# Kernel tuning notes

Measured on AMD Instinct MI355X. Metric: run time of the kernel, lower is better.

The kernel has to match this reference:

```python
import jax, jax.numpy as jnp
import numpy as np

INPUT_DIM = 1024
UNITS = 1024

def setup_inputs() -> dict:
    key = jax.random.key(0)
    ks = jax.random.split(key, 7)
    B, S = 4, 2048
    x = jax.random.normal(ks[0], (B, S, INPUT_DIM), dtype=jnp.float32)
    # nn.Linear weights stored as [out, in]; biases [out]
    scale = 1.0 / np.sqrt(INPUT_DIM)
    Wq = jax.random.uniform(ks[1], (UNITS, INPUT_DIM), jnp.float32, -scale, scale)
    bq = jax.random.uniform(ks[2], (UNITS,), jnp.float32, -scale, scale)
    Wk = jax.random.uniform(ks[3], (UNITS, INPUT_DIM), jnp.float32, -scale, scale)
    bk = jax.random.uniform(ks[4], (UNITS,), jnp.float32, -scale, scale)
    Wv = jax.random.uniform(ks[5], (UNITS, INPUT_DIM), jnp.float32, -scale, scale)
    bv = jax.random.uniform(ks[6], (UNITS,), jnp.float32, -scale, scale)
    return {"x": x, "Wq": Wq, "bq": bq, "Wk": Wk, "bk": bk, "Wv": Wv, "bv": bv}

def reference(x, Wq, bq, Wk, bk, Wv, bv):
    # Q/K/V projections: [B,S,D] @ [D,U]
    Q = jnp.einsum('bsd,ud->bsu', x, Wq) + bq
    K = jnp.einsum('bsd,ud->bsu', x, Wk) + bk
    V = jnp.einsum('bsd,ud->bsu', x, Wv) + bv
    scores = jnp.einsum('bqu,bku->bqk', Q, K) / jnp.sqrt(jnp.float32(UNITS))
    attn = jax.nn.softmax(scores, axis=-1)
    return jnp.einsum('bqk,bku->bqu', attn, V)
```

## Files before the change

### kernel.cpp

```cpp
#include <hip/hip_runtime.h>
#include <cstdint>
#include <cstddef>


typedef unsigned short ushort_t;
typedef unsigned char u8;
typedef __attribute__((ext_vector_type(4))) short short4v;
typedef __attribute__((ext_vector_type(8))) short short8;
typedef __attribute__((ext_vector_type(4))) float f32x4;

#define AS1 __attribute__((address_space(1)))
#define AS3 __attribute__((address_space(3)))

__device__ __forceinline__ ushort_t f2bf(float f) {
    unsigned int u = __float_as_uint(f);
    u += 0x7FFFu + ((u >> 16) & 1u);
    return (ushort_t)(u >> 16);
}
__device__ __forceinline__ float bf2f(ushort_t b) {
    return __uint_as_float(((unsigned)b) << 16);
}

__device__ __forceinline__ void async_ld16(const void* g, unsigned lds_off) {
    __builtin_amdgcn_global_load_lds((const AS1 void*)(uintptr_t)g,
                                     (AS3 void*)(uintptr_t)lds_off,
                                     16, 0, 0);
}

__global__ __launch_bounds__(512, 2) void qkv_gemm(
    const ushort_t* __restrict__ X,
    const ushort_t* __restrict__ W0, const ushort_t* __restrict__ W1,
    const ushort_t* __restrict__ W2,
    const float* __restrict__ b0, const float* __restrict__ b1,
    const float* __restrict__ b2,
    u8* __restrict__ Q8, u8* __restrict__ K8, ushort_t* __restrict__ Vt)
{
    __shared__ __align__(16) ushort_t As[128 * 64];
    __shared__ __align__(16) ushort_t Bs[3][128 * 64];

    const int tid  = threadIdx.x;
    const int wave = tid >> 6;
    const int lane = tid & 63;

    const int m0 = blockIdx.y * 128;
    const int n0 = blockIdx.x * 128;
    const int wm = (wave >> 2) * 64;
    const int wn = (wave & 3) * 32;

    const unsigned ldsA = (unsigned)(uintptr_t)&As[0];
    const unsigned ldsB = (unsigned)(uintptr_t)&Bs[0][0];
    constexpr unsigned BSTEP = 128 * 64 * 2;

    const int srow = (wave << 3) + (lane >> 3);
    const int cd   = ((lane & 7) - (lane >> 3)) & 7;
    const ushort_t* gX  = X  + (size_t)(m0 + srow) * 1024 + cd * 8;
    const ushort_t* gW0 = W0 + (size_t)(n0 + srow) * 1024 + cd * 8;
    const ushort_t* gW1 = W1 + (size_t)(n0 + srow) * 1024 + cd * 8;
    const ushort_t* gW2 = W2 + (size_t)(n0 + srow) * 1024 + cd * 8;
    const unsigned lw = (wave << 10);

    const int frow = lane & 15;
    const int fg   = lane >> 4;

    f32x4 acc[3][4][2] = {};

    for (int k0 = 0; k0 < 1024; k0 += 64) {
        if (k0) __syncthreads();
#pragma unroll
        for (int c = 0; c < 2; ++c) {
            const size_t ro = (size_t)c * 64;
            async_ld16(gX  + ro * 1024, ldsA + c * 8192 + lw);
            async_ld16(gW0 + ro * 1024, ldsB + 0 * BSTEP + c * 8192 + lw);
            async_ld16(gW1 + ro * 1024, ldsB + 1 * BSTEP + c * 8192 + lw);
            async_ld16(gW2 + ro * 1024, ldsB + 2 * BSTEP + c * 8192 + lw);
        }
        gX += 64; gW0 += 64; gW1 += 64; gW2 += 64;
        __syncthreads();

#pragma unroll
        for (int t = 0; t < 2; ++t) {
            const int ck = (t << 2) + fg;
            short8 af[4], bf[2];
#pragma unroll
            for (int i = 0; i < 4; ++i) {
                const int row = wm + i * 16 + frow;
                af[i] = *(const short8*)&As[row * 64 + (((ck + row) & 7) << 3)];
            }
#pragma unroll
            for (int o = 0; o < 3; ++o) {
#pragma unroll
                for (int j = 0; j < 2; ++j) {
                    const int row = wn + j * 16 + frow;
                    bf[j] = *(const short8*)&Bs[o][row * 64 + (((ck + row) & 7) << 3)];
                }
#pragma unroll
                for (int i = 0; i < 4; ++i)
#pragma unroll
                    for (int j = 0; j < 2; ++j)
                        acc[o][i][j] = __builtin_amdgcn_mfma_f32_16x16x32_bf16(
                            af[i], bf[j], acc[o][i][j], 0, 0, 0);
            }
        }
    }

    const int r0 = (lane >> 4) << 2;
    const int c0 = lane & 15;
#pragma unroll
    for (int o = 0; o < 2; ++o) {
        u8* C = (o == 0) ? Q8 : K8;
        const float* bia = (o == 0) ? b0 : b1;
#pragma unroll
        for (int i = 0; i < 4; ++i) {
#pragma unroll
            for (int j = 0; j < 2; ++j) {
                const int n = n0 + wn + j * 16 + c0;
                const float bn = bia[n];
                const int p0 = __builtin_amdgcn_cvt_pk_fp8_f32(
                    acc[o][i][j][0] + bn, acc[o][i][j][1] + bn, 0, false);
                const int p1 = __builtin_amdgcn_cvt_pk_fp8_f32(
                    acc[o][i][j][2] + bn, acc[o][i][j][3] + bn, 0, false);
                const size_t mb = (size_t)(m0 + wm + i * 16 + r0);
                C[(mb + 0) * 1024 + n] = (u8)(p0 & 0xFF);
                C[(mb + 1) * 1024 + n] = (u8)((p0 >> 8) & 0xFF);
                C[(mb + 2) * 1024 + n] = (u8)(p1 & 0xFF);
                C[(mb + 3) * 1024 + n] = (u8)((p1 >> 8) & 0xFF);
            }
        }
    }
#pragma unroll
    for (int i = 0; i < 4; ++i) {
#pragma unroll
        for (int j = 0; j < 2; ++j) {
            const int n = n0 + wn + j * 16 + c0;
            const int m = m0 + wm + i * 16 + r0;
            const float bn = b2[n];
            short4v pk;
#pragma unroll
            for (int r = 0; r < 4; ++r)
                pk[r] = (short)f2bf(acc[2][i][j][r] + bn);
            *(short4v*)&Vt[(size_t)n * 8192 + m] = pk;
        }
    }
}

__global__ __launch_bounds__(256, 2) void qk_fp8(
    const u8* __restrict__ Q8, const u8* __restrict__ K8,
    ushort_t* __restrict__ Sc)
{
    __shared__ __align__(16) u8 As[128 * 64];
    __shared__ __align__(16) u8 Bs[128 * 64];

    const int tid  = threadIdx.x;
    const int wave = tid >> 6;
    const int lane = tid & 63;

    const u8* A = Q8 + (size_t)blockIdx.z * 2048 * 1024;
    const u8* B = K8 + (size_t)blockIdx.z * 2048 * 1024;

    const int m0 = blockIdx.y * 128;
    const int n0 = blockIdx.x * 128;
    const int wm = (wave >> 1) * 64;
    const int wn = (wave & 1) * 64;

    const unsigned ldsA = (unsigned)(uintptr_t)&As[0];
    const unsigned ldsB = (unsigned)(uintptr_t)&Bs[0];

    const int srow = (wave << 4) + (lane >> 2);
    const int cd   = ((lane & 3) - srow) & 3;
    const u8* gA = A + (size_t)(m0 + srow) * 1024 + cd * 16;
    const u8* gB = B + (size_t)(n0 + srow) * 1024 + cd * 16;
    const unsigned lw = (wave << 10);

    const int frow = lane & 15;
    const int fg   = lane >> 4;

    f32x4 acc[4][4] = {};

    for (int k0 = 0; k0 < 1024; k0 += 64) {
        if (k0) __syncthreads();
        async_ld16(gA,             ldsA + lw);
        async_ld16(gA + 64 * 1024, ldsA + 4096 + lw);
        async_ld16(gB,             ldsB + lw);
        async_ld16(gB + 64 * 1024, ldsB + 4096 + lw);
        gA += 64; gB += 64;
        __syncthreads();

#pragma unroll
        for (int t = 0; t < 2; ++t) {
            const int ck = (t << 1) + (fg >> 1);
            const int io = (fg & 1) << 3;
            long long af[4], bf[4];
#pragma unroll
            for (int i = 0; i < 4; ++i) {
                const int row = wm + i * 16 + frow;
                af[i] = *(const long long*)&As[row * 64 + (((ck + row) & 3) << 4) + io];
            }
#pragma unroll
            for (int j = 0; j < 4; ++j) {
                const int row = wn + j * 16 + frow;
                bf[j] = *(const long long*)&Bs[row * 64 + (((ck + row) & 3) << 4) + io];
            }
#pragma unroll
            for (int i = 0; i < 4; ++i)
#pragma unroll
                for (int j = 0; j < 4; ++j)
                    acc[i][j] = __builtin_amdgcn_mfma_f32_16x16x32_fp8_fp8(
                        af[i], bf[j], acc[i][j], 0, 0, 0);
        }
    }

    const int r0 = (lane >> 4) << 2;
    const int c0 = lane & 15;
    ushort_t* C = Sc + (size_t)blockIdx.z * 2048 * 2048;
#pragma unroll
    for (int i = 0; i < 4; ++i)
#pragma unroll
        for (int j = 0; j < 4; ++j) {
            const int n = n0 + wn + j * 16 + c0;
#pragma unroll
            for (int r = 0; r < 4; ++r) {
                const int m = m0 + wm + i * 16 + r0 + r;
                C[(size_t)m * 2048 + n] = f2bf(__expf(acc[i][j][r] * 0.03125f));
            }
        }
}

__global__ __launch_bounds__(256, 2) void pv_gemm(
    const ushort_t* __restrict__ A, const ushort_t* __restrict__ B0,
    float* __restrict__ C0)
{
    constexpr int BK = 64, P = 8;

    __shared__ __align__(16) ushort_t As[128 * BK];
    __shared__ __align__(16) ushort_t Bs[128 * BK];
    __shared__ float rs[128];

    const int tid  = threadIdx.x;
    const int wave = tid >> 6;
    const int lane = tid & 63;

    A += (size_t)blockIdx.z * 2048 * 2048;
    const ushort_t* B = B0 + (size_t)blockIdx.z * 2048;

    const int m0 = blockIdx.y * 128;
    const int n0 = blockIdx.x * 128;
    const int wm = (wave >> 1) * 64;
    const int wn = (wave & 1) * 64;

    const unsigned ldsA = (unsigned)(uintptr_t)&As[0];
    const unsigned ldsB = (unsigned)(uintptr_t)&Bs[0];

    const int srow = wave * 8 + lane / P;
    const int cd   = ((lane & (P - 1)) - srow) & (P - 1);
    const ushort_t* gA = A + (size_t)(m0 + srow) * 2048 + cd * 8;
    const ushort_t* gB = B + (size_t)(n0 + srow) * 8192 + cd * 8;
    const unsigned lw = (wave << 10);

    const int frow = lane & 15;
    const int fg   = lane >> 4;

    f32x4 acc[4][4] = {};
    float rsacc[4] = {0.f, 0.f, 0.f, 0.f};

    for (int k0 = 0; k0 < 2048; k0 += BK) {
        if (k0) __syncthreads();
#pragma unroll
        for (int c = 0; c < 4; ++c) {
            const size_t ro = (size_t)c * 32;
            async_ld16(gA + ro * 2048, ldsA + c * 4096 + lw);
            async_ld16(gB + ro * 8192, ldsB + c * 4096 + lw);
        }
        gA += BK; gB += BK;
        __syncthreads();

#pragma unroll
        for (int t = 0; t < 2; ++t) {
            const int pa = (((t << 2) + fg + frow) & (P - 1)) << 3;
            short8 af[4], bf[4];
#pragma unroll
            for (int i = 0; i < 4; ++i)
                af[i] = *(const short8*)&As[(wm + i * 16 + frow) * BK + pa];
            if (wn == 0) {
#pragma unroll
                for (int i = 0; i < 4; ++i)
#pragma unroll
                    for (int e = 0; e < 8; ++e)
                        rsacc[i] += bf2f((ushort_t)af[i][e]);
            }
#pragma unroll
            for (int j = 0; j < 4; ++j)
                bf[j] = *(const short8*)&Bs[(wn + j * 16 + frow) * BK + pa];
#pragma unroll
            for (int i = 0; i < 4; ++i)
#pragma unroll
                for (int j = 0; j < 4; ++j)
                    acc[i][j] = __builtin_amdgcn_mfma_f32_16x16x32_bf16(
                        af[i], bf[j], acc[i][j], 0, 0, 0);
        }
    }

    if (wn == 0) {
#pragma unroll
        for (int i = 0; i < 4; ++i) {
            float s = rsacc[i];
            s += __shfl_xor(s, 16, 64);
            s += __shfl_xor(s, 32, 64);
            rs[wm + i * 16 + frow] = s;
        }
    }
    __syncthreads();

    const int r0 = (lane >> 4) << 2;
    const int c0 = lane & 15;
    float* C = C0 + (size_t)blockIdx.z * 2048 * 1024;
#pragma unroll
    for (int i = 0; i < 4; ++i) {
        float bm[4];
#pragma unroll
        for (int r = 0; r < 4; ++r)
            bm[r] = 1.0f / rs[wm + i * 16 + r0 + r];
#pragma unroll
        for (int j = 0; j < 4; ++j) {
            const int n = n0 + wn + j * 16 + c0;
#pragma unroll
            for (int r = 0; r < 4; ++r) {
                const int m = m0 + wm + i * 16 + r0 + r;
                C[(size_t)m * 1024 + n] = acc[i][j][r] * bm[r];
            }
        }
    }
}

__global__ __launch_bounds__(256) void cvt_all(
    const float* __restrict__ x,  const float* __restrict__ wq,
    const float* __restrict__ wk, const float* __restrict__ wv,
    ushort_t* __restrict__ xb,  ushort_t* __restrict__ wqb,
    ushort_t* __restrict__ wkb, ushort_t* __restrict__ wvb)
{
    const int b = blockIdx.x;
    const float* src; ushort_t* dst; size_t base;
    if (b < 4096)      { src = x;  dst = xb;  base = (size_t)b * 2048; }
    else if (b < 4608) { src = wq; dst = wqb; base = (size_t)(b - 4096) * 2048; }
    else if (b < 5120) { src = wk; dst = wkb; base = (size_t)(b - 4608) * 2048; }
    else               { src = wv; dst = wvb; base = (size_t)(b - 5120) * 2048; }
    const size_t i = base + threadIdx.x * 8;
    const f32x4 a = *(const f32x4*)(src + i);
    const f32x4 c = *(const f32x4*)(src + i + 4);
    short8 o;
    o[0] = (short)f2bf(a[0]); o[1] = (short)f2bf(a[1]);
    o[2] = (short)f2bf(a[2]); o[3] = (short)f2bf(a[3]);
    o[4] = (short)f2bf(c[0]); o[5] = (short)f2bf(c[1]);
    o[6] = (short)f2bf(c[2]); o[7] = (short)f2bf(c[3]);
    *(short8*)(dst + i) = o;
}

extern "C" void kernel_launch(void* const* d_in, const int* in_sizes, int n_in,
                              void* d_out, int out_size, void* d_ws, size_t ws_size,
                              hipStream_t stream)
{
    const float* x  = (const float*)d_in[0];
    const float* Wq = (const float*)d_in[1];
    const float* bq = (const float*)d_in[2];
    const float* Wk = (const float*)d_in[3];
    const float* bk = (const float*)d_in[4];
    const float* Wv = (const float*)d_in[5];
    const float* bv = (const float*)d_in[6];
    float* out = (float*)d_out;

    char* ws = (char*)d_ws;
    const size_t MB = 1ull << 20;
    ushort_t* Xb  = (ushort_t*)(ws);
    ushort_t* Wqb = (ushort_t*)(ws + 16 * MB);
    ushort_t* Wkb = (ushort_t*)(ws + 18 * MB);
    ushort_t* Wvb = (ushort_t*)(ws + 20 * MB);
    u8*       Q8  = (u8*)(ws + 32 * MB);
    u8*       K8  = (u8*)(ws + 40 * MB);
    ushort_t* Vt  = (ushort_t*)(ws + 64 * MB);
    ushort_t* Sc  = (ushort_t*)(ws);

    cvt_all<<<dim3(5632), dim3(256), 0, stream>>>(
        x, Wq, Wk, Wv, Xb, Wqb, Wkb, Wvb);

    qkv_gemm<<<dim3(8, 64), dim3(512), 0, stream>>>(
        Xb, Wqb, Wkb, Wvb, bq, bk, bv, Q8, K8, Vt);

    qk_fp8<<<dim3(16, 16, 4), dim3(256), 0, stream>>>(Q8, K8, Sc);

    pv_gemm<<<dim3(8, 16, 4), dim3(256), 0, stream>>>(Sc, Vt, out);
}
```

Measured before the change: 257.0 us.

## Merge four kernels into one persistent kernel with global atomic barriers

Replaces the four separate launches (convert, QKV GEMM, QK^T fp8, PV GEMM) with one persistent 256-block kernel that walks through the phases, separated by a software grid barrier built on an atomic counter. Tile shapes change too: QK uses 128x256 tiles and PV uses 512-thread blocks with 128x128 tiles. The aim is to remove launch gaps and tail effects between kernels. In exchange it adds barrier spin cost, limits each phase to 256 blocks (2 tiles each), and depends on all 256 blocks being co-resident, or the barrier deadlocks.

```diff
diff --git a/kernel.cpp b/kernel.cpp
--- a/kernel.cpp
+++ b/kernel.cpp
@@ -20,338 +20,342 @@
 __device__ __forceinline__ float bf2f(ushort_t b) {
     return __uint_as_float(((unsigned)b) << 16);
 }
-
 __device__ __forceinline__ void async_ld16(const void* g, unsigned lds_off) {
     __builtin_amdgcn_global_load_lds((const AS1 void*)(uintptr_t)g,
-                                     (AS3 void*)(uintptr_t)lds_off,
-                                     16, 0, 0);
-}
-
-__global__ __launch_bounds__(512, 2) void qkv_gemm(
-    const ushort_t* __restrict__ X,
-    const ushort_t* __restrict__ W0, const ushort_t* __restrict__ W1,
-    const ushort_t* __restrict__ W2,
-    const float* __restrict__ b0, const float* __restrict__ b1,
-    const float* __restrict__ b2,
-    u8* __restrict__ Q8, u8* __restrict__ K8, ushort_t* __restrict__ Vt)
+                                     (AS3 void*)(uintptr_t)lds_off, 16, 0, 0);
+}
+__device__ __forceinline__ void cvt8(const float* __restrict__ s,
+                                     ushort_t* __restrict__ d, size_t i) {
+    const f32x4 a = *(const f32x4*)(s + i);
+    const f32x4 b = *(const f32x4*)(s + i + 4);
+    short8 o;
+    o[0] = (short)f2bf(a[0]); o[1] = (short)f2bf(a[1]);
+    o[2] = (short)f2bf(a[2]); o[3] = (short)f2bf(a[3]);
+    o[4] = (short)f2bf(b[0]); o[5] = (short)f2bf(b[1]);
+    o[6] = (short)f2bf(b[2]); o[7] = (short)f2bf(b[3]);
+    *(short8*)(d + i) = o;
+}
+
+__device__ __forceinline__ void gsync(int* bar, int target) {
+    __syncthreads();
+    if (threadIdx.x == 0) {
+        __hip_atomic_fetch_add(bar, 1, __ATOMIC_RELEASE,
+                               __HIP_MEMORY_SCOPE_AGENT);
+        while (__hip_atomic_load(bar, __ATOMIC_ACQUIRE,
+                                 __HIP_MEMORY_SCOPE_AGENT) < target) {
+            __builtin_amdgcn_s_sleep(8);
+        }
+    }
+    __syncthreads();
+}
+
+__global__ __launch_bounds__(512, 4) void fa_persist(
+    const float* __restrict__ x,
+    const float* __restrict__ Wq, const float* __restrict__ bq,
+    const float* __restrict__ Wk, const float* __restrict__ bk,
+    const float* __restrict__ Wv, const float* __restrict__ bv,
+    float* __restrict__ out,
+    ushort_t* __restrict__ Xb, ushort_t* __restrict__ Wqb,
+    ushort_t* __restrict__ Wkb, ushort_t* __restrict__ Wvb,
+    u8* __restrict__ Q8, u8* __restrict__ K8,
+    ushort_t* __restrict__ Vt, ushort_t* __restrict__ Sc,
+    int* __restrict__ bar)
 {
-    __shared__ __align__(16) ushort_t As[128 * 64];
-    __shared__ __align__(16) ushort_t Bs[3][128 * 64];
+    __shared__ __align__(16) char smem[65536];
 
     const int tid  = threadIdx.x;
     const int wave = tid >> 6;
     const int lane = tid & 63;
-
-    const int m0 = blockIdx.y * 128;
-    const int n0 = blockIdx.x * 128;
-    const int wm = (wave >> 2) * 64;
-    const int wn = (wave & 3) * 32;
-
-    const unsigned ldsA = (unsigned)(uintptr_t)&As[0];
-    const unsigned ldsB = (unsigned)(uintptr_t)&Bs[0][0];
-    constexpr unsigned BSTEP = 128 * 64 * 2;
-
-    const int srow = (wave << 3) + (lane >> 3);
-    const int cd   = ((lane & 7) - (lane >> 3)) & 7;
-    const ushort_t* gX  = X  + (size_t)(m0 + srow) * 1024 + cd * 8;
-    const ushort_t* gW0 = W0 + (size_t)(n0 + srow) * 1024 + cd * 8;
-    const ushort_t* gW1 = W1 + (size_t)(n0 + srow) * 1024 + cd * 8;
-    const ushort_t* gW2 = W2 + (size_t)(n0 + srow) * 1024 + cd * 8;
-    const unsigned lw = (wave << 10);
-
+    const int blk  = blockIdx.x;
     const int frow = lane & 15;
     const int fg   = lane >> 4;
-
-    f32x4 acc[3][4][2] = {};
-
-    for (int k0 = 0; k0 < 1024; k0 += 64) {
-        if (k0) __syncthreads();
-#pragma unroll
-        for (int c = 0; c < 2; ++c) {
-            const size_t ro = (size_t)c * 64;
-            async_ld16(gX  + ro * 1024, ldsA + c * 8192 + lw);
-            async_ld16(gW0 + ro * 1024, ldsB + 0 * BSTEP + c * 8192 + lw);
-            async_ld16(gW1 + ro * 1024, ldsB + 1 * BSTEP + c * 8192 + lw);
-            async_ld16(gW2 + ro * 1024, ldsB + 2 * BSTEP + c * 8192 + lw);
+    const int r0   = (lane >> 4) << 2;
+    const int c0   = lane & 15;
+
+    {
+        const int gt = blk * 512 + tid;
+#pragma unroll
+        for (int it = 0; it < 8; ++it)
+            cvt8(x, Xb, ((size_t)gt + (size_t)it * 131072) * 8);
+        cvt8(Wq, Wqb, (size_t)gt * 8);
+        cvt8(Wk, Wkb, (size_t)gt * 8);
+        cvt8(Wv, Wvb, (size_t)gt * 8);
+    }
+    gsync(bar, 256);
+
+    {
+        ushort_t* As = (ushort_t*)smem;
+        ushort_t* Bs = (ushort_t*)(smem + 16384);
+        const unsigned ldsA = (unsigned)(uintptr_t)As;
+        const unsigned ldsB = (unsigned)(uintptr_t)Bs;
+        constexpr unsigned BSTEP = 128 * 64 * 2;
+
+        for (int ti = 0; ti < 2; ++ti) {
+            const int t  = blk + ti * 256;
+            const int bx = t & 7, by = t >> 3;
+            const int m0 = by * 128, n0 = bx * 128;
+            const int wm = (wave >> 2) * 64;
+            const int wn = (wave & 3) * 32;
+
+            const int srow = (wave << 3) + (lane >> 3);
+            const int cd   = ((lane & 7) - (lane >> 3)) & 7;
+            const ushort_t* gX  = Xb  + (size_t)(m0 + srow) * 1024 + cd * 8;
+            const ushort_t* gW0 = Wqb + (size_t)(n0 + srow) * 1024 + cd * 8;
+            const ushort_t* gW1 = Wkb + (size_t)(n0 + srow) * 1024 + cd * 8;
+            const ushort_t* gW2 = Wvb + (size_t)(n0 + srow) * 1024 + cd * 8;
+            const unsigned lw = (wave << 10);
+
+            f32x4 acc[3][4][2] = {};
+
+            for (int k0 = 0; k0 < 1024; k0 += 64) {
+                __syncthreads();
+#pragma unroll
+                for (int c = 0; c < 2; ++c) {
+                    const size_t ro = (size_t)c * 64;
+                    async_ld16(gX  + ro * 1024, ldsA + c * 8192 + lw);
+                    async_ld16(gW0 + ro * 1024, ldsB + 0 * BSTEP + c * 8192 + lw);
+                    async_ld16(gW1 + ro * 1024, ldsB + 1 * BSTEP + c * 8192 + lw);
+                    async_ld16(gW2 + ro * 1024, ldsB + 2 * BSTEP + c * 8192 + lw);
+                }
+                gX += 64; gW0 += 64; gW1 += 64; gW2 += 64;
+                __syncthreads();
+
+#pragma unroll
+                for (int tt = 0; tt < 2; ++tt) {
+                    const int ck = (tt << 2) + fg;
+                    short8 af[4], bf[2];
+#pragma unroll
+                    for (int i = 0; i < 4; ++i) {
+                        const int row = wm + i * 16 + frow;
+                        af[i] = *(const short8*)&As[row * 64 + (((ck + row) & 7) << 3)];
+                    }
+#pragma unroll
+                    for (int o = 0; o < 3; ++o) {
+#pragma unroll
+                        for (int j = 0; j < 2; ++j) {
+                            const int row = wn + j * 16 + frow;
+                            bf[j] = *(const short8*)&Bs[(size_t)o * 128 * 64 +
+                                       row * 64 + (((ck + row) & 7) << 3)];
+                        }
+#pragma unroll
+                        for (int i = 0; i < 4; ++i)
+#pragma unroll
+                            for (int j = 0; j < 2; ++j)
+                                acc[o][i][j] = __builtin_amdgcn_mfma_f32_16x16x32_bf16(
+                                    af[i], bf[j], acc[o][i][j], 0, 0, 0);
+                    }
+                }
+            }
+
+#pragma unroll
+            for (int o = 0; o < 2; ++o) {
+                u8* C = (o == 0) ? Q8 : K8;
+                const float* bia = (o == 0) ? bq : bk;
+#pragma unroll
+                for (int i = 0; i < 4; ++i) {
+#pragma unroll
+                    for (int j = 0; j < 2; ++j) {
+                        const int n = n0 + wn + j * 16 + c0;
+                        const float bn = bia[n];
+                        const int p0 = __builtin_amdgcn_cvt_pk_fp8_f32(
+                            acc[o][i][j][0] + bn, acc[o][i][j][1] + bn, 0, false);
+                        const int p1 = __builtin_amdgcn_cvt_pk_fp8_f32(
+                            acc[o][i][j][2] + bn, acc[o][i][j][3] + bn, 0, false);
+                        const size_t mb = (size_t)(m0 + wm + i * 16 + r0);
+                        C[(mb + 0) * 1024 + n] = (u8)(p0 & 0xFF);
+                        C[(mb + 1) * 1024 + n] = (u8)((p0 >> 8) & 0xFF);
+                        C[(mb + 2) * 1024 + n] = (u8)(p1 & 0xFF);
+                        C[(mb + 3) * 1024 + n] = (u8)((p1 >> 8) & 0xFF);
+                    }
+                }
+            }
+#pragma unroll
+            for (int i = 0; i < 4; ++i) {
+#pragma unroll
+                for (int j = 0; j < 2; ++j) {
+                    const int n = n0 + wn + j * 16 + c0;
+                    const int m = m0 + wm + i * 16 + r0;
+                    const float bn = bv[n];
+                    short4v pk;
+#pragma unroll
+                    for (int r = 0; r < 4; ++r)
+                        pk[r] = (short)f2bf(acc[2][i][j][r] + bn);
+                    *(short4v*)&Vt[(size_t)n * 8192 + m] = pk;
+                }
+            }
         }
-        gX += 64; gW0 += 64; gW1 += 64; gW2 += 64;
-        __syncthreads();
-
-#pragma unroll
-        for (int t = 0; t < 2; ++t) {
-            const int ck = (t << 2) + fg;
-            short8 af[4], bf[2];
+    }
+    gsync(bar, 512);
+
+    {
+        u8* As8 = (u8*)smem;
+        u8* Bs8 = (u8*)(smem + 8192);
+        const unsigned ldsA = (unsigned)(uintptr_t)As8;
+        const unsigned ldsB = (unsigned)(uintptr_t)Bs8;
+
+        for (int ti = 0; ti < 2; ++ti) {
+            const int t  = blk + ti * 256;
+            const int z  = t >> 7;
+            const int rr = t & 127;
+            const int m0 = (rr >> 3) * 128;
+            const int n0 = (rr & 7) * 256;
+            const int wm = (wave >> 2) * 64;
+            const int wn = (wave & 3) * 64;
+
+            const u8* A = Q8 + (size_t)z * 2048 * 1024;
+            const u8* B = K8 + (size_t)z * 2048 * 1024;
+
+            const int srow = (wave << 4) + (lane >> 2);
+            const int cd   = ((lane & 3) - srow) & 3;
+            const u8* gA = A + (size_t)(m0 + srow) * 1024 + cd * 16;
+            const u8* gB = B + (size_t)(n0 + srow) * 1024 + cd * 16;
+            const unsigned lw = (wave << 10);
+
+            f32x4 acc[4][4] = {};
+
+            for (int k0 = 0; k0 < 1024; k0 += 64) {
+                __syncthreads();
+                async_ld16(gA,              ldsA + lw);
+                async_ld16(gB,              ldsB + lw);
+                async_ld16(gB + 128 * 1024, ldsB + 8192 + lw);
+                gA += 64; gB += 64;
+                __syncthreads();
+
+#pragma unroll
+                for (int tt = 0; tt < 2; ++tt) {
+                    const int ck = (tt << 1) + (fg >> 1);
+                    const int io = (fg & 1) << 3;
+                    long long af[4], bf[4];
+#pragma unroll
+                    for (int i = 0; i < 4; ++i) {
+                        const int row = wm + i * 16 + frow;
+                        af[i] = *(const long long*)&As8[row * 64 + (((ck + row) & 3) << 4) + io];
+                    }
+#pragma unroll
+                    for (int j = 0; j < 4; ++j) {
+                        const int row = wn + j * 16 + frow;
+                        bf[j] = *(const long long*)&Bs8[row * 64 + (((ck + row) & 3) << 4) + io];
+                    }
+#pragma unroll
+                    for (int i = 0; i < 4; ++i)
+#pragma unroll
+                        for (int j = 0; j < 4; ++j)
+                            acc[i][j] = __builtin_amdgcn_mfma_f32_16x16x32_fp8_fp8(
+                                af[i], bf[j], acc[i][j], 0, 0, 0);
+                }
+            }
+
+            ushort_t* C = Sc + (size_t)z * 2048 * 2048;
+#pragma unroll
+            for (int i = 0; i < 4; ++i)
+#pragma unroll
+                for (int j = 0; j < 4; ++j) {
+                    const int n = n0 + wn + j * 16 + c0;
+#pragma unroll
+                    for (int r = 0; r < 4; ++r) {
+                        const int m = m0 + wm + i * 16 + r0 + r;
+                        C[(size_t)m * 2048 + n] = f2bf(__expf(acc[i][j][r] * 0.03125f));
+                    }
+                }
+        }
+    }
+    gsync(bar, 768);
+
+    {
+        ushort_t* As = (ushort_t*)smem;
+        ushort_t* Bs = (ushort_t*)(smem + 16384);
+        float*    rs = (float*)(smem + 32768);
+        const unsigned ldsA = (unsigned)(uintptr_t)As;
+        const unsigned ldsB = (unsigned)(uintptr_t)Bs;
+
+        for (int ti = 0; ti < 2; ++ti) {
+            const int t  = blk + ti * 256;
+            const int z  = t >> 7;
+            const int rr = t & 127;
+            const int m0 = (rr >> 3) * 128;
+            const int n0 = (rr & 7) * 128;
+            const int wm = (wave >> 2) * 64;
+            const int wn = (wave & 3) * 32;
+
+            const ushort_t* A = Sc + (size_t)z * 2048 * 2048;
+            const ushort_t* B = Vt + (size_t)z * 2048;
+
+            const int srow = (wave << 3) + (lane >> 3);
+            const int cd   = ((lane & 7) - (lane >> 3)) & 7;
+            const ushort_t* gA = A + (size_t)(m0 + srow) * 2048 + cd * 8;
+            const ushort_t* gB = B + (size_t)(n0 + srow) * 8192 + cd * 8;
+            const unsigned lw = (wave << 10);
+
+            f32x4 acc[4][2] = {};
+            float rsacc[4] = {0.f, 0.f, 0.f, 0.f};
+
+            for (int k0 = 0; k0 < 2048; k0 += 64) {
+                __syncthreads();
+#pragma unroll
+                for (int c = 0; c < 2; ++c) {
+                    const size_t ro = (size_t)c * 64;
+                    async_ld16(gA + ro * 2048, ldsA + c * 8192 + lw);
+                    async_ld16(gB + ro * 8192, ldsB + c * 8192 + lw);
+                }
+                gA += 64; gB += 64;
+                __syncthreads();
+
+#pragma unroll
+                for (int tt = 0; tt < 2; ++tt) {
+                    const int pa = (((tt << 2) + fg + frow) & 7) << 3;
+                    short8 af[4], bf[2];
+#pragma unroll
+                    for (int i = 0; i < 4; ++i)
+                        af[i] = *(const short8*)&As[(wm + i * 16 + frow) * 64 + pa];
+                    if (wn == 0) {
+#pragma unroll
+                        for (int i = 0; i < 4; ++i)
+#pragma unroll
+                            for (int e = 0; e < 8; ++e)
+                                rsacc[i] += bf2f((ushort_t)af[i][e]);
+                    }
+#pragma unroll
+                    for (int j = 0; j < 2; ++j)
+                        bf[j] = *(const short8*)&Bs[(wn + j * 16 + frow) * 64 + pa];
+#pragma unroll
+                    for (int i = 0; i < 4; ++i)
+#pragma unroll
+                        for (int j = 0; j < 2; ++j)
+                            acc[i][j] = __builtin_amdgcn_mfma_f32_16x16x32_bf16(
+                                af[i], bf[j], acc[i][j], 0, 0, 0);
+                }
+            }
+
+            if (wn == 0) {
+#pragma unroll
+                for (int i = 0; i < 4; ++i) {
+                    float s = rsacc[i];
+                    s += __shfl_xor(s, 16, 64);
+                    s += __shfl_xor(s, 32, 64);
+                    rs[wm + i * 16 + frow] = s;
+                }
+            }
+            __syncthreads();
+
+            float* C = out + (size_t)z * 2048 * 1024;
 #pragma unroll
             for (int i = 0; i < 4; ++i) {
-                const int row = wm + i * 16 + frow;
-                af[i] = *(const short8*)&As[row * 64 + (((ck + row) & 7) << 3)];
-            }
-#pragma unroll
-            for (int o = 0; o < 3; ++o) {
+                float bm[4];
+#pragma unroll
+                for (int r = 0; r < 4; ++r)
+                    bm[r] = 1.0f / rs[wm + i * 16 + r0 + r];
 #pragma unroll
                 for (int j = 0; j < 2; ++j) {
-                    const int row = wn + j * 16 + frow;
-                    bf[j] = *(const short8*)&Bs[o][row * 64 + (((ck + row) & 7) << 3)];
-                }
-#pragma unroll
-                for (int i = 0; i < 4; ++i)
-#pragma unroll
-                    for (int j = 0; j < 2; ++j)
-                        acc[o][i][j] = __builtin_amdgcn_mfma_f32_16x16x32_bf16(
-                            af[i], bf[j], acc[o][i][j], 0, 0, 0);
+                    const int n = n0 + wn + j * 16 + c0;
+#pragma unroll
+                    for (int r = 0; r < 4; ++r) {
+                        const int m = m0 + wm + i * 16 + r0 + r;
+                        C[(size_t)m * 1024 + n] = acc[i][j][r] * bm[r];
+                    }
+                }
             }
         }
     }
-
-    const int r0 = (lane >> 4) << 2;
-    const int c0 = lane & 15;
-#pragma unroll
-    for (int o = 0; o < 2; ++o) {
-        u8* C = (o == 0) ? Q8 : K8;
-        const float* bia = (o == 0) ? b0 : b1;
-#pragma unroll
-        for (int i = 0; i < 4; ++i) {
-#pragma unroll
-            for (int j = 0; j < 2; ++j) {
-                const int n = n0 + wn + j * 16 + c0;
-                const float bn = bia[n];
-                const int p0 = __builtin_amdgcn_cvt_pk_fp8_f32(
-                    acc[o][i][j][0] + bn, acc[o][i][j][1] + bn, 0, false);
-                const int p1 = __builtin_amdgcn_cvt_pk_fp8_f32(
-                    acc[o][i][j][2] + bn, acc[o][i][j][3] + bn, 0, false);
-                const size_t mb = (size_t)(m0 + wm + i * 16 + r0);
-                C[(mb + 0) * 1024 + n] = (u8)(p0 & 0xFF);
-                C[(mb + 1) * 1024 + n] = (u8)((p0 >> 8) & 0xFF);
-                C[(mb + 2) * 1024 + n] = (u8)(p1 & 0xFF);
-                C[(mb + 3) * 1024 + n] = (u8)((p1 >> 8) & 0xFF);
-            }
-        }
-    }
-#pragma unroll
-    for (int i = 0; i < 4; ++i) {
-#pragma unroll
-        for (int j = 0; j < 2; ++j) {
-            const int n = n0 + wn + j * 16 + c0;
-            const int m = m0 + wm + i * 16 + r0;
-            const float bn = b2[n];
-            short4v pk;
-#pragma unroll
-            for (int r = 0; r < 4; ++r)
-                pk[r] = (short)f2bf(acc[2][i][j][r] + bn);
-            *(short4v*)&Vt[(size_t)n * 8192 + m] = pk;
-        }
-    }
-}
-
-__global__ __launch_bounds__(256, 2) void qk_fp8(
-    const u8* __restrict__ Q8, const u8* __restrict__ K8,
-    ushort_t* __restrict__ Sc)
-{
-    __shared__ __align__(16) u8 As[128 * 64];
-    __shared__ __align__(16) u8 Bs[128 * 64];
-
-    const int tid  = threadIdx.x;
-    const int wave = tid >> 6;
-    const int lane = tid & 63;
-
-    const u8* A = Q8 + (size_t)blockIdx.z * 2048 * 1024;
-    const u8* B = K8 + (size_t)blockIdx.z * 2048 * 1024;
-
-    const int m0 = blockIdx.y * 128;
-    const int n0 = blockIdx.x * 128;
-    const int wm = (wave >> 1) * 64;
-    const int wn = (wave & 1) * 64;
-
-    const unsigned ldsA = (unsigned)(uintptr_t)&As[0];
-    const unsigned ldsB = (unsigned)(uintptr_t)&Bs[0];
-
-    const int srow = (wave << 4) + (lane >> 2);
-    const int cd   = ((lane & 3) - srow) & 3;
-    const u8* gA = A + (size_t)(m0 + srow) * 1024 + cd * 16;
-    const u8* gB = B + (size_t)(n0 + srow) * 1024 + cd * 16;
-    const unsigned lw = (wave << 10);
-
-    const int frow = lane & 15;
-    const int fg   = lane >> 4;
-
-    f32x4 acc[4][4] = {};
-
-    for (int k0 = 0; k0 < 1024; k0 += 64) {
-        if (k0) __syncthreads();
-        async_ld16(gA,             ldsA + lw);
-        async_ld16(gA + 64 * 1024, ldsA + 4096 + lw);
-        async_ld16(gB,             ldsB + lw);
-        async_ld16(gB + 64 * 1024, ldsB + 4096 + lw);
-        gA += 64; gB += 64;
-        __syncthreads();
-
-#pragma unroll
-        for (int t = 0; t < 2; ++t) {
-            const int ck = (t << 1) + (fg >> 1);
-            const int io = (fg & 1) << 3;
-            long long af[4], bf[4];
-#pragma unroll
-            for (int i = 0; i < 4; ++i) {
-                const int row = wm + i * 16 + frow;
-                af[i] = *(const long long*)&As[row * 64 + (((ck + row) & 3) << 4) + io];
-            }
-#pragma unroll
-            for (int j = 0; j < 4; ++j) {
-                const int row = wn + j * 16 + frow;
-                bf[j] = *(const long long*)&Bs[row * 64 + (((ck + row) & 3) << 4) + io];
-            }
-#pragma unroll
-            for (int i = 0; i < 4; ++i)
-#pragma unroll
-                for (int j = 0; j < 4; ++j)
-                    acc[i][j] = __builtin_amdgcn_mfma_f32_16x16x32_fp8_fp8(
-                        af[i], bf[j], acc[i][j], 0, 0, 0);
-        }
-    }
-
-    const int r0 = (lane >> 4) << 2;
-    const int c0 = lane & 15;
-    ushort_t* C = Sc + (size_t)blockIdx.z * 2048 * 2048;
-#pragma unroll
-    for (int i = 0; i < 4; ++i)
-#pragma unroll
-        for (int j = 0; j < 4; ++j) {
-            const int n = n0 + wn + j * 16 + c0;
-#pragma unroll
-            for (int r = 0; r < 4; ++r) {
-                const int m = m0 + wm + i * 16 + r0 + r;
-                C[(size_t)m * 2048 + n] = f2bf(__expf(acc[i][j][r] * 0.03125f));
-            }
-        }
-}
-
-__global__ __launch_bounds__(256, 2) void pv_gemm(
-    const ushort_t* __restrict__ A, const ushort_t* __restrict__ B0,
-    float* __restrict__ C0)
-{
-    constexpr int BK = 64, P = 8;
-
-    __shared__ __align__(16) ushort_t As[128 * BK];
-    __shared__ __align__(16) ushort_t Bs[128 * BK];
-    __shared__ float rs[128];
-
-    const int tid  = threadIdx.x;
-    const int wave = tid >> 6;
-    const int lane = tid & 63;
-
-    A += (size_t)blockIdx.z * 2048 * 2048;
-    const ushort_t* B = B0 + (size_t)blockIdx.z * 2048;
-
-    const int m0 = blockIdx.y * 128;
-    const int n0 = blockIdx.x * 128;
-    const int wm = (wave >> 1) * 64;
-    const int wn = (wave & 1) * 64;
-
-    const unsigned ldsA = (unsigned)(uintptr_t)&As[0];
-    const unsigned ldsB = (unsigned)(uintptr_t)&Bs[0];
-
-    const int srow = wave * 8 + lane / P;
-    const int cd   = ((lane & (P - 1)) - srow) & (P - 1);
-    const ushort_t* gA = A + (size_t)(m0 + srow) * 2048 + cd * 8;
-    const ushort_t* gB = B + (size_t)(n0 + srow) * 8192 + cd * 8;
-    const unsigned lw = (wave << 10);
-
-    const int frow = lane & 15;
-    const int fg   = lane >> 4;
-
-    f32x4 acc[4][4] = {};
-    float rsacc[4] = {0.f, 0.f, 0.f, 0.f};
-
-    for (int k0 = 0; k0 < 2048; k0 += BK) {
-        if (k0) __syncthreads();
-#pragma unroll
-        for (int c = 0; c < 4; ++c) {
-            const size_t ro = (size_t)c * 32;
-            async_ld16(gA + ro * 2048, ldsA + c * 4096 + lw);
-            async_ld16(gB + ro * 8192, ldsB + c * 4096 + lw);
-        }
-        gA += BK; gB += BK;
-        __syncthreads();
-
-#pragma unroll
-        for (int t = 0; t < 2; ++t) {
-            const int pa = (((t << 2) + fg + frow) & (P - 1)) << 3;
-            short8 af[4], bf[4];
-#pragma unroll
-            for (int i = 0; i < 4; ++i)
-                af[i] = *(const short8*)&As[(wm + i * 16 + frow) * BK + pa];
-            if (wn == 0) {
-#pragma unroll
-                for (int i = 0; i < 4; ++i)
-#pragma unroll
-                    for (int e = 0; e < 8; ++e)
-                        rsacc[i] += bf2f((ushort_t)af[i][e]);
-            }
-#pragma unroll
-            for (int j = 0; j < 4; ++j)
-                bf[j] = *(const short8*)&Bs[(wn + j * 16 + frow) * BK + pa];
-#pragma unroll
-            for (int i = 0; i < 4; ++i)
-#pragma unroll
-                for (int j = 0; j < 4; ++j)
-                    acc[i][j] = __builtin_amdgcn_mfma_f32_16x16x32_bf16(
-                        af[i], bf[j], acc[i][j], 0, 0, 0);
-        }
-    }
-
-    if (wn == 0) {
-#pragma unroll
-        for (int i = 0; i < 4; ++i) {
-            float s = rsacc[i];
-            s += __shfl_xor(s, 16, 64);
-            s += __shfl_xor(s, 32, 64);
-            rs[wm + i * 16 + frow] = s;
-        }
-    }
-    __syncthreads();
-
-    const int r0 = (lane >> 4) << 2;
-    const int c0 = lane & 15;
-    float* C = C0 + (size_t)blockIdx.z * 2048 * 1024;
-#pragma unroll
-    for (int i = 0; i < 4; ++i) {
-        float bm[4];
-#pragma unroll
-        for (int r = 0; r < 4; ++r)
-            bm[r] = 1.0f / rs[wm + i * 16 + r0 + r];
-#pragma unroll
-        for (int j = 0; j < 4; ++j) {
-            const int n = n0 + wn + j * 16 + c0;
-#pragma unroll
-            for (int r = 0; r < 4; ++r) {
-                const int m = m0 + wm + i * 16 + r0 + r;
-                C[(size_t)m * 1024 + n] = acc[i][j][r] * bm[r];
-            }
-        }
-    }
-}
-
-__global__ __launch_bounds__(256) void cvt_all(
-    const float* __restrict__ x,  const float* __restrict__ wq,
-    const float* __restrict__ wk, const float* __restrict__ wv,
-    ushort_t* __restrict__ xb,  ushort_t* __restrict__ wqb,
-    ushort_t* __restrict__ wkb, ushort_t* __restrict__ wvb)
-{
-    const int b = blockIdx.x;
-    const float* src; ushort_t* dst; size_t base;
-    if (b < 4096)      { src = x;  dst = xb;  base = (size_t)b * 2048; }
-    else if (b < 4608) { src = wq; dst = wqb; base = (size_t)(b - 4096) * 2048; }
-    else if (b < 5120) { src = wk; dst = wkb; base = (size_t)(b - 4608) * 2048; }
-    else               { src = wv; dst = wvb; base = (size_t)(b - 5120) * 2048; }
-    const size_t i = base + threadIdx.x * 8;
-    const f32x4 a = *(const f32x4*)(src + i);
-    const f32x4 c = *(const f32x4*)(src + i + 4);
-    short8 o;
-    o[0] = (short)f2bf(a[0]); o[1] = (short)f2bf(a[1]);
-    o[2] = (short)f2bf(a[2]); o[3] = (short)f2bf(a[3]);
-    o[4] = (short)f2bf(c[0]); o[5] = (short)f2bf(c[1]);
-    o[6] = (short)f2bf(c[2]); o[7] = (short)f2bf(c[3]);
-    *(short8*)(dst + i) = o;
 }
 
 extern "C" void kernel_launch(void* const* d_in, const int* in_sizes, int n_in,
@@ -375,16 +379,12 @@
     ushort_t* Wvb = (ushort_t*)(ws + 20 * MB);
     u8*       Q8  = (u8*)(ws + 32 * MB);
     u8*       K8  = (u8*)(ws + 40 * MB);
+    int*      bar = (int*)(ws + 48 * MB);
     ushort_t* Vt  = (ushort_t*)(ws + 64 * MB);
     ushort_t* Sc  = (ushort_t*)(ws);
 
-    cvt_all<<<dim3(5632), dim3(256), 0, stream>>>(
-        x, Wq, Wk, Wv, Xb, Wqb, Wkb, Wvb);
-
-    qkv_gemm<<<dim3(8, 64), dim3(512), 0, stream>>>(
-        Xb, Wqb, Wkb, Wvb, bq, bk, bv, Q8, K8, Vt);
-
-    qk_fp8<<<dim3(16, 16, 4), dim3(256), 0, stream>>>(Q8, K8, Sc);
-
-    pv_gemm<<<dim3(8, 16, 4), dim3(256), 0, stream>>>(Sc, Vt, out);
-}
+    hipMemsetAsync(bar, 0, sizeof(int), stream);
+    fa_persist<<<dim3(256), dim3(512), 0, stream>>>(
+        x, Wq, bq, Wk, bk, Wv, bv, out,
+        Xb, Wqb, Wkb, Wvb, Q8, K8, Vt, Sc, bar);
+}
```

After: 458.6 us. +78.5%, slower.
